# Kernel optimization log

Measured on AMD Instinct MI355X. Metric: run time of the kernel, lower is better.

## Reference

```python
import jax, jax.numpy as jnp
import numpy as np
import math

EMBED = 1024
HEADS = 16
HEAD_DIM = EMBED // HEADS


def setup_inputs() -> dict:
    key = jax.random.key(0)
    k1, k2, k3 = jax.random.split(key, 3)
    B, C, N = 2, EMBED, 2048
    x = jax.random.normal(k1, (B, C, N), dtype=jnp.float32)
    # Conv1d(kernel_size=1, bias=False) weights, stored as [out_ch, in_ch]
    fan = 1.0 / math.sqrt(EMBED)
    w_qkv = jax.random.uniform(k2, (3 * EMBED, EMBED), dtype=jnp.float32, minval=-fan, maxval=fan)
    w_out = jax.random.uniform(k3, (EMBED, EMBED), dtype=jnp.float32, minval=-fan, maxval=fan)
    return {"x": x, "w_qkv": w_qkv, "w_out": w_out}


def reference(x, w_qkv, w_out):
    B, C, N = x.shape
    H, HD = HEADS, HEAD_DIM
    # 1x1 conv == channel matmul: [B, 3E, N]
    qkv = jnp.einsum('oc,bcn->bon', w_qkv, x)
    # permute -> [B, N, 3E]; reshape splits 3E as (H, 3*HD) per original code
    qkv = qkv.transpose(0, 2, 1).reshape(B, N, H, 3 * HD)
    qkv = qkv.transpose(0, 2, 1, 3)  # [B, H, N, 3*HD]
    q, k, v = jnp.split(qkv, 3, axis=-1)  # each [B, H, N, HD]
    scale = 1.0 / math.sqrt(HD)
    scores = jnp.einsum('bhnd,bhmd->bhnm', q, k) * scale
    weight = jax.nn.softmax(scores, axis=-1)
    vals = jnp.einsum('bhnm,bhmd->bhnd', weight, v)
    vals = vals.transpose(0, 2, 1, 3).reshape(B, N, C)  # [B, N, C]
    y = jnp.einsum('oc,bnc->bon', w_out, vals)  # [B, C, N]
    return y
```

## Files before the change

kernel.cpp:

```cpp
#include <hip/hip_runtime.h>
#include <stdint.h>

typedef unsigned short u16;
typedef __attribute__((ext_vector_type(8))) short bf16x8;
typedef __attribute__((ext_vector_type(4))) float f32x4;

#define NSEQ  2048
#define EMBED 1024
#define NHEAD 16
#define HDIM  64
#define QSCALE 0.1803368801111204f

__device__ __forceinline__ u16 f2bf(float f) {
  uint32_t u = __builtin_bit_cast(uint32_t, f);
  u += 0x7fffu + ((u >> 16) & 1u);
  return (u16)(u >> 16);
}

__device__ __forceinline__ uint32_t cvtpk(float a, float b) {
  uint32_t r;
  asm("v_cvt_pk_bf16_f32 %0, %1, %2" : "=v"(r) : "v"(a), "v"(b));
  return r;
}

__device__ __forceinline__ void gl_lds16(const void* g, void* l) {
  __builtin_amdgcn_global_load_lds(
      (const __attribute__((address_space(1))) void*)g,
      (__attribute__((address_space(3))) void*)l, 16, 0, 0);
}

struct alignas(8) us4 { u16 a, b, c, d; };

__global__ __launch_bounds__(256)
void convertw(const float* __restrict__ wq, const float* __restrict__ wo,
              u16* __restrict__ oq, u16* __restrict__ oo) {
  int idx = blockIdx.x * 256 + threadIdx.x;
  const float* src;
  u16* dst;
  if (idx < 786432) { src = wq; dst = oq; }
  else { idx -= 786432; src = wo; dst = oo; }
  f32x4 v = ((const f32x4*)src)[idx];
  us4 r;
  r.a = f2bf(v[0]); r.b = f2bf(v[1]); r.c = f2bf(v[2]); r.d = f2bf(v[3]);
  ((us4*)dst)[idx] = r;
}

__global__ __launch_bounds__(256)
void transpose_x(const float* __restrict__ x, u16* __restrict__ xT) {
  __shared__ float tile[32][33];
  const int b = blockIdx.z;
  const int n0 = blockIdx.x * 32, c0 = blockIdx.y * 32;
  const int tx = threadIdx.x & 31, ty = threadIdx.x >> 5;
  const float* xb = x + (size_t)b * EMBED * NSEQ;
  #pragma unroll
  for (int k = 0; k < 4; ++k)
    tile[ty + k * 8][tx] = xb[(size_t)(c0 + ty + k * 8) * NSEQ + n0 + tx];
  __syncthreads();
  u16* xTb = xT + (size_t)b * NSEQ * EMBED;
  #pragma unroll
  for (int k = 0; k < 4; ++k)
    xTb[(size_t)(n0 + ty + k * 8) * EMBED + c0 + tx] = f2bf(tile[tx][ty + k * 8]);
}

template<int EPI>
__global__ __launch_bounds__(256, 2)
void gemm_bt(const u16* __restrict__ A, const u16* __restrict__ Bm,
             u16* __restrict__ o_q, u16* __restrict__ o_k, u16* __restrict__ o_vt,
             float* __restrict__ o_f)
{
  __shared__ u16 lA[128 * 64];
  __shared__ u16 lB[128 * 64];
  const int t  = threadIdx.x;
  const int w  = t >> 6;
  const int l  = t & 63;
  const int lr = l & 15, lh = l >> 4;
  const int wm = w >> 1, wn = w & 1;
  const int bz = blockIdx.z;
  const int m0 = blockIdx.x * 128;
  const int n0 = blockIdx.y * 128;

  const u16* Ab = A  + (EPI == 0 ? (size_t)bz * NSEQ * EMBED : (size_t)0);
  const u16* Bb = Bm + (EPI == 0 ? (size_t)0 : (size_t)bz * NSEQ * EMBED);

  f32x4 acc[4][4];
  #pragma unroll
  for (int i = 0; i < 4; ++i)
    #pragma unroll
    for (int j = 0; j < 4; ++j)
      acc[i][j] = (f32x4){0.f, 0.f, 0.f, 0.f};

  const int srow = t >> 3;
  const int slot = t & 7;
  char* ldsA = (char*)lA + (w << 10);
  char* ldsB = (char*)lB + (w << 10);

  for (int k0 = 0; k0 < EMBED; k0 += 64) {
    __syncthreads();
    #pragma unroll
    for (int i = 0; i < 4; ++i) {
      const int row = i * 32 + srow;
      const int sc  = ((slot * 16) ^ ((row & 7) << 4)) >> 1;
      gl_lds16(Ab + (size_t)(m0 + row) * EMBED + k0 + sc, ldsA + i * 4096);
      gl_lds16(Bb + (size_t)(n0 + row) * EMBED + k0 + sc, ldsB + i * 4096);
    }
    __syncthreads();
    #pragma unroll
    for (int kk = 0; kk < 2; ++kk) {
      bf16x8 af[4], bfr[4];
      #pragma unroll
      for (int mr = 0; mr < 4; ++mr) {
        const int row = wm * 64 + mr * 16 + lr;
        const int c2  = (kk * 64 + lh * 16) ^ ((row & 7) << 4);
        af[mr] = *(const bf16x8*)((const char*)lA + row * 128 + c2);
      }
      #pragma unroll
      for (int nc = 0; nc < 4; ++nc) {
        const int row = wn * 64 + nc * 16 + lr;
        const int c2  = (kk * 64 + lh * 16) ^ ((row & 7) << 4);
        bfr[nc] = *(const bf16x8*)((const char*)lB + row * 128 + c2);
      }
      #pragma unroll
      for (int mr = 0; mr < 4; ++mr)
        #pragma unroll
        for (int nc = 0; nc < 4; ++nc)
          acc[mr][nc] = __builtin_amdgcn_mfma_f32_16x16x32_bf16(
              af[mr], bfr[nc], acc[mr][nc], 0, 0, 0);
    }
  }

  if constexpr (EPI == 0) {
    #pragma unroll
    for (int mr = 0; mr < 4; ++mr) {
      #pragma unroll
      for (int nc = 0; nc < 4; ++nc) {
        const int o  = n0 + wn * 64 + nc * 16 + lr;
        const int h  = o / 192;
        const int rr = o - h * 192;
        const size_t bh = (size_t)bz * NHEAD + h;
        #pragma unroll
        for (int r = 0; r < 4; ++r) {
          const int n = m0 + wm * 64 + mr * 16 + lh * 4 + r;
          if (rr < 64)       o_q [(bh * NSEQ + n) * HDIM + rr]         = f2bf(acc[mr][nc][r] * QSCALE);
          else if (rr < 128) o_k [(bh * NSEQ + n) * HDIM + (rr - 64)]  = f2bf(acc[mr][nc][r]);
          else               o_vt[(bh * HDIM + (rr - 128)) * NSEQ + n] = f2bf(acc[mr][nc][r]);
        }
      }
    }
  } else {
    #pragma unroll
    for (int mr = 0; mr < 4; ++mr)
      #pragma unroll
      for (int nc = 0; nc < 4; ++nc)
        #pragma unroll
        for (int r = 0; r < 4; ++r) {
          const int o = m0 + wm * 64 + mr * 16 + lh * 4 + r;
          const int n = n0 + wn * 64 + nc * 16 + lr;
          o_f[((size_t)bz * EMBED + o) * NSEQ + n] = acc[mr][nc][r];
        }
  }
}

__global__ __launch_bounds__(256, 4)
void attn(const u16* __restrict__ Q, const u16* __restrict__ K,
          const u16* __restrict__ Vt, u16* __restrict__ vals)
{
  __shared__ u16 lK[2][64 * 64], lV[2][64 * 64], lQP[64 * 64];
  const int t  = threadIdx.x;
  const int w  = t >> 6, l = t & 63;
  const int lr = l & 15, lh = l >> 4;
  const int bid = blockIdx.x;
  const int s   = bid >> 3;
  const int bh  = (bid & 7) + 8 * (s >> 5);
  const int q0  = (s & 31) * 64;
  const int b  = bh >> 4, h = bh & 15;
  const size_t qk0 = (size_t)bh * NSEQ * HDIM;
  const size_t vt0 = (size_t)bh * HDIM * NSEQ;
  const int srow = t >> 3, slot = t & 7;
  const int swzr = (lr & 7) << 4;
  char* const pbase = (char*)lQP + (w << 11) + lr * 128;

  #pragma unroll
  for (int i = 0; i < 2; ++i) {
    const int row = i * 32 + srow;
    const int sc  = ((slot * 16) ^ ((row & 7) << 4)) >> 1;
    gl_lds16(Q + qk0 + (size_t)(q0 + row) * HDIM + sc,
             (char*)lQP + i * 4096 + (w << 10));
    gl_lds16(K + qk0 + (size_t)row * HDIM + sc,
             (char*)lK[0] + i * 4096 + (w << 10));
    gl_lds16(Vt + vt0 + (size_t)row * NSEQ + sc,
             (char*)lV[0] + i * 4096 + (w << 10));
  }
  __syncthreads();

  bf16x8 qf[2];
  {
    const int qrow = w * 16 + lr;
    #pragma unroll
    for (int kk = 0; kk < 2; ++kk)
      qf[kk] = *(const bf16x8*)((const char*)lQP + qrow * 128 +
                                ((kk * 64 + lh * 16) ^ ((qrow & 7) << 4)));
  }

  f32x4 accO[4];
  #pragma unroll
  for (int i = 0; i < 4; ++i) accO[i] = (f32x4){0.f, 0.f, 0.f, 0.f};
  float m = -1e30f, lsum = 0.f;
  int cur = 0;

  for (int j0 = 0; j0 < NSEQ; j0 += 64) {
    const int jn = j0 + 64;
    if (jn < NSEQ) {
      char* nk = (char*)lK[cur ^ 1];
      char* nv = (char*)lV[cur ^ 1];
      #pragma unroll
      for (int i = 0; i < 2; ++i) {
        const int row = i * 32 + srow;
        const int sc  = ((slot * 16) ^ ((row & 7) << 4)) >> 1;
        gl_lds16(K  + qk0 + (size_t)(jn + row) * HDIM + sc, nk + i * 4096 + (w << 10));
        gl_lds16(Vt + vt0 + (size_t)row * NSEQ + jn + sc,   nv + i * 4096 + (w << 10));
      }
    }
    const char* kb = (const char*)lK[cur];
    const char* vb = (const char*)lV[cur];

    f32x4 accS[4];
    #pragma unroll
    for (int f = 0; f < 4; ++f) accS[f] = (f32x4){0.f, 0.f, 0.f, 0.f};
    __builtin_amdgcn_s_setprio(1);
    #pragma unroll
    for (int kk = 0; kk < 2; ++kk)
      #pragma unroll
      for (int f = 0; f < 4; ++f) {
        const int row = f * 16 + lr;
        const int c2  = (kk * 64 + lh * 16) ^ ((row & 7) << 4);
        bf16x8 kf = *(const bf16x8*)(kb + row * 128 + c2);
        accS[f] = __builtin_amdgcn_mfma_f32_16x16x32_bf16(kf, qf[kk], accS[f], 0, 0, 0);
      }
    __builtin_amdgcn_s_setprio(0);

    float fm[4];
    #pragma unroll
    for (int f = 0; f < 4; ++f)
      fm[f] = fmaxf(fmaxf(accS[f][0], accS[f][1]), fmaxf(accS[f][2], accS[f][3]));
    float tm = fmaxf(fmaxf(fm[0], fm[1]), fmaxf(fm[2], fm[3]));
    tm = fmaxf(tm, __shfl_xor(tm, 16, 64));
    tm = fmaxf(tm, __shfl_xor(tm, 32, 64));

    if (tm > m + 8.f) {
      const float al = exp2f(m - tm);
      lsum *= al;
      #pragma unroll
      for (int fd = 0; fd < 4; ++fd)
        #pragma unroll
        for (int r = 0; r < 4; ++r)
          accO[fd][r] *= al;
      m = tm;
    }

    float psum = 0.f;
    #pragma unroll
    for (int f = 0; f < 4; ++f) {
      const float e0 = exp2f(accS[f][0] - m);
      const float e1 = exp2f(accS[f][1] - m);
      const float e2 = exp2f(accS[f][2] - m);
      const float e3 = exp2f(accS[f][3] - m);
      psum += (e0 + e1) + (e2 + e3);
      uint2 pw;
      pw.x = cvtpk(e0, e1);
      pw.y = cvtpk(e2, e3);
      *(uint2*)(pbase + ((f * 32 + lh * 8) ^ swzr)) = pw;
    }
    psum += __shfl_xor(psum, 16, 64);
    psum += __shfl_xor(psum, 32, 64);
    lsum += psum;

    __builtin_amdgcn_s_setprio(1);
    #pragma unroll
    for (int kk = 0; kk < 2; ++kk) {
      bf16x8 pf = *(const bf16x8*)(pbase + ((kk * 64 + lh * 16) ^ swzr));
      #pragma unroll
      for (int fd = 0; fd < 4; ++fd) {
        const int row = fd * 16 + lr;
        const int c2  = (kk * 64 + lh * 16) ^ ((row & 7) << 4);
        bf16x8 vf = *(const bf16x8*)(vb + row * 128 + c2);
        accO[fd] = __builtin_amdgcn_mfma_f32_16x16x32_bf16(vf, pf, accO[fd], 0, 0, 0);
      }
    }
    __builtin_amdgcn_s_setprio(0);

    __syncthreads();
    cur ^= 1;
  }

  const float rl = 1.0f / lsum;
  const int n = q0 + w * 16 + lr;
  #pragma unroll
  for (int fd = 0; fd < 4; ++fd) {
    uint2 ow;
    ow.x = cvtpk(accO[fd][0] * rl, accO[fd][1] * rl);
    ow.y = cvtpk(accO[fd][2] * rl, accO[fd][3] * rl);
    const int c = h * HDIM + fd * 16 + lh * 4;
    *(uint2*)(vals + ((size_t)b * NSEQ + n) * EMBED + c) = ow;
  }
}

extern "C" void kernel_launch(void* const* d_in, const int* in_sizes, int n_in,
                              void* d_out, int out_size, void* d_ws, size_t ws_size,
                              hipStream_t stream) {
  const float* x    = (const float*)d_in[0];
  const float* wqkv = (const float*)d_in[1];
  const float* wout = (const float*)d_in[2];
  float* y = (float*)d_out;
  char* ws = (char*)d_ws;

  u16* b_wqkv = (u16*)(ws);
  u16* b_wout = (u16*)(ws + 6291456);
  u16* b_xT   = (u16*)(ws + 8388608);
  u16* b_Q    = (u16*)(ws + 16777216);
  u16* b_K    = (u16*)(ws + 25165824);
  u16* b_Vt   = (u16*)(ws + 33554432);
  u16* b_vals = (u16*)(ws + 41943040);

  convertw<<<4096, 256, 0, stream>>>(wqkv, wout, b_wqkv, b_wout);
  transpose_x<<<dim3(64, 32, 2), 256, 0, stream>>>(x, b_xT);
  gemm_bt<0><<<dim3(16, 24, 2), 256, 0, stream>>>(b_xT, b_wqkv, b_Q, b_K, b_Vt, nullptr);
  attn<<<1024, 256, 0, stream>>>(b_Q, b_K, b_Vt, b_vals);
  gemm_bt<1><<<dim3(8, 16, 2), 256, 0, stream>>>(b_wout, b_vals, nullptr, nullptr, nullptr, y);
}
```

Before: 215.2 us.

## Restructure attention loop with static double-buffer, swizzle GEMM blocks, halve out-proj M tile

```diff
diff --git a/kernel.cpp b/kernel.cpp
--- a/kernel.cpp
+++ b/kernel.cpp
@@ -62,13 +62,13 @@
     xTb[(size_t)(n0 + ty + k * 8) * EMBED + c0 + tx] = f2bf(tile[tx][ty + k * 8]);
 }
 
-template<int EPI>
+template<int EPI, int MR>
 __global__ __launch_bounds__(256, 2)
 void gemm_bt(const u16* __restrict__ A, const u16* __restrict__ Bm,
              u16* __restrict__ o_q, u16* __restrict__ o_k, u16* __restrict__ o_vt,
              float* __restrict__ o_f)
 {
-  __shared__ u16 lA[128 * 64];
+  __shared__ u16 lA[MR * 32 * 64];
   __shared__ u16 lB[128 * 64];
   const int t  = threadIdx.x;
   const int w  = t >> 6;
@@ -76,15 +76,18 @@
   const int lr = l & 15, lh = l >> 4;
   const int wm = w >> 1, wn = w & 1;
   const int bz = blockIdx.z;
-  const int m0 = blockIdx.x * 128;
-  const int n0 = blockIdx.y * 128;
+  const int NT  = (EPI == 0 ? 384 : 256);
+  const int c   = blockIdx.x + 16 * blockIdx.y;
+  const int swz = (c & 7) * (NT / 8) + (c >> 3);
+  const int m0  = (swz & 15) * (MR * 32);
+  const int n0  = (swz >> 4) * 128;
 
   const u16* Ab = A  + (EPI == 0 ? (size_t)bz * NSEQ * EMBED : (size_t)0);
   const u16* Bb = Bm + (EPI == 0 ? (size_t)0 : (size_t)bz * NSEQ * EMBED);
 
-  f32x4 acc[4][4];
-  #pragma unroll
-  for (int i = 0; i < 4; ++i)
+  f32x4 acc[MR][4];
+  #pragma unroll
+  for (int i = 0; i < MR; ++i)
     #pragma unroll
     for (int j = 0; j < 4; ++j)
       acc[i][j] = (f32x4){0.f, 0.f, 0.f, 0.f};
@@ -97,19 +100,24 @@
   for (int k0 = 0; k0 < EMBED; k0 += 64) {
     __syncthreads();
     #pragma unroll
+    for (int i = 0; i < MR; ++i) {
+      const int row = i * 32 + srow;
+      const int sc  = ((slot * 16) ^ ((row & 7) << 4)) >> 1;
+      gl_lds16(Ab + (size_t)(m0 + row) * EMBED + k0 + sc, ldsA + i * 4096);
+    }
+    #pragma unroll
     for (int i = 0; i < 4; ++i) {
       const int row = i * 32 + srow;
       const int sc  = ((slot * 16) ^ ((row & 7) << 4)) >> 1;
-      gl_lds16(Ab + (size_t)(m0 + row) * EMBED + k0 + sc, ldsA + i * 4096);
       gl_lds16(Bb + (size_t)(n0 + row) * EMBED + k0 + sc, ldsB + i * 4096);
     }
     __syncthreads();
     #pragma unroll
     for (int kk = 0; kk < 2; ++kk) {
-      bf16x8 af[4], bfr[4];
-      #pragma unroll
-      for (int mr = 0; mr < 4; ++mr) {
-        const int row = wm * 64 + mr * 16 + lr;
+      bf16x8 af[MR], bfr[4];
+      #pragma unroll
+      for (int mr = 0; mr < MR; ++mr) {
+        const int row = wm * (MR * 16) + mr * 16 + lr;
         const int c2  = (kk * 64 + lh * 16) ^ ((row & 7) << 4);
         af[mr] = *(const bf16x8*)((const char*)lA + row * 128 + c2);
       }
@@ -120,7 +128,7 @@
         bfr[nc] = *(const bf16x8*)((const char*)lB + row * 128 + c2);
       }
       #pragma unroll
-      for (int mr = 0; mr < 4; ++mr)
+      for (int mr = 0; mr < MR; ++mr)
         #pragma unroll
         for (int nc = 0; nc < 4; ++nc)
           acc[mr][nc] = __builtin_amdgcn_mfma_f32_16x16x32_bf16(
@@ -130,7 +138,7 @@
 
   if constexpr (EPI == 0) {
     #pragma unroll
-    for (int mr = 0; mr < 4; ++mr) {
+    for (int mr = 0; mr < MR; ++mr) {
       #pragma unroll
       for (int nc = 0; nc < 4; ++nc) {
         const int o  = n0 + wn * 64 + nc * 16 + lr;
@@ -139,7 +147,7 @@
         const size_t bh = (size_t)bz * NHEAD + h;
         #pragma unroll
         for (int r = 0; r < 4; ++r) {
-          const int n = m0 + wm * 64 + mr * 16 + lh * 4 + r;
+          const int n = m0 + wm * (MR * 16) + mr * 16 + lh * 4 + r;
           if (rr < 64)       o_q [(bh * NSEQ + n) * HDIM + rr]         = f2bf(acc[mr][nc][r] * QSCALE);
           else if (rr < 128) o_k [(bh * NSEQ + n) * HDIM + (rr - 64)]  = f2bf(acc[mr][nc][r]);
           else               o_vt[(bh * HDIM + (rr - 128)) * NSEQ + n] = f2bf(acc[mr][nc][r]);
@@ -148,12 +156,12 @@
     }
   } else {
     #pragma unroll
-    for (int mr = 0; mr < 4; ++mr)
+    for (int mr = 0; mr < MR; ++mr)
       #pragma unroll
       for (int nc = 0; nc < 4; ++nc)
         #pragma unroll
         for (int r = 0; r < 4; ++r) {
-          const int o = m0 + wm * 64 + mr * 16 + lh * 4 + r;
+          const int o = m0 + wm * (MR * 16) + mr * 16 + lh * 4 + r;
           const int n = n0 + wn * 64 + nc * 16 + lr;
           o_f[((size_t)bz * EMBED + o) * NSEQ + n] = acc[mr][nc][r];
         }
@@ -179,17 +187,87 @@
   const int swzr = (lr & 7) << 4;
   char* const pbase = (char*)lQP + (w << 11) + lr * 128;
 
+#define STAGE(J, KB, VB) do {                                                  \
+    _Pragma("unroll")                                                          \
+    for (int i_ = 0; i_ < 2; ++i_) {                                           \
+      const int row_ = i_ * 32 + srow;                                         \
+      const int sc_  = ((slot * 16) ^ ((row_ & 7) << 4)) >> 1;                 \
+      gl_lds16(K  + qk0 + (size_t)((J) + row_) * HDIM + sc_,                   \
+               (char*)(KB) + i_ * 4096 + (w << 10));                           \
+      gl_lds16(Vt + vt0 + (size_t)row_ * NSEQ + (J) + sc_,                     \
+               (char*)(VB) + i_ * 4096 + (w << 10));                           \
+    }                                                                          \
+  } while (0)
+
+#define ATILE(KB, VB) do {                                                     \
+    f32x4 accS[4];                                                             \
+    _Pragma("unroll")                                                          \
+    for (int f_ = 0; f_ < 4; ++f_) accS[f_] = (f32x4){0.f, 0.f, 0.f, 0.f};     \
+    __builtin_amdgcn_s_setprio(1);                                             \
+    _Pragma("unroll")                                                          \
+    for (int kk_ = 0; kk_ < 2; ++kk_)                                          \
+      _Pragma("unroll")                                                        \
+      for (int f_ = 0; f_ < 4; ++f_) {                                         \
+        const int row_ = f_ * 16 + lr;                                         \
+        const int c2_  = (kk_ * 64 + lh * 16) ^ swzr;                          \
+        bf16x8 kf_ = *(const bf16x8*)((const char*)(KB) + row_ * 128 + c2_);   \
+        accS[f_] = __builtin_amdgcn_mfma_f32_16x16x32_bf16(kf_, qf[kk_],       \
+                                                           accS[f_], 0, 0, 0);\
+      }                                                                        \
+    __builtin_amdgcn_s_setprio(0);                                             \
+    float fm0_ = fmaxf(fmaxf(accS[0][0], accS[0][1]), fmaxf(accS[0][2], accS[0][3])); \
+    float fm1_ = fmaxf(fmaxf(accS[1][0], accS[1][1]), fmaxf(accS[1][2], accS[1][3])); \
+    float fm2_ = fmaxf(fmaxf(accS[2][0], accS[2][1]), fmaxf(accS[2][2], accS[2][3])); \
+    float fm3_ = fmaxf(fmaxf(accS[3][0], accS[3][1]), fmaxf(accS[3][2], accS[3][3])); \
+    float tm_ = fmaxf(fmaxf(fm0_, fm1_), fmaxf(fm2_, fm3_));                   \
+    tm_ = fmaxf(tm_, __shfl_xor(tm_, 16, 64));                                 \
+    tm_ = fmaxf(tm_, __shfl_xor(tm_, 32, 64));                                 \
+    if (tm_ > m + 8.f) {            \
+      const float al_ = exp2f(m - tm_);                                        \
+      lsum *= al_;                                                             \
+      _Pragma("unroll")                                                        \
+      for (int fd_ = 0; fd_ < 4; ++fd_)                                        \
+        _Pragma("unroll")                                                      \
+        for (int r_ = 0; r_ < 4; ++r_) accO[fd_][r_] *= al_;                   \
+      m = tm_;                                                                 \
+    }                                                                          \
+    _Pragma("unroll")                                                          \
+    for (int f_ = 0; f_ < 4; ++f_) {                                           \
+      const float e0_ = exp2f(accS[f_][0] - m);                                \
+      const float e1_ = exp2f(accS[f_][1] - m);                                \
+      const float e2_ = exp2f(accS[f_][2] - m);                                \
+      const float e3_ = exp2f(accS[f_][3] - m);                                \
+      lsum += (e0_ + e1_) + (e2_ + e3_);   \
+      uint2 pw_;                                                               \
+      pw_.x = cvtpk(e0_, e1_);                                                 \
+      pw_.y = cvtpk(e2_, e3_);                                                 \
+      *(uint2*)(pbase + ((f_ * 32 + lh * 8) ^ swzr)) = pw_;                    \
+    }                                                                          \
+    __builtin_amdgcn_s_setprio(1);                                             \
+    _Pragma("unroll")                                                          \
+    for (int kk_ = 0; kk_ < 2; ++kk_) {                                        \
+      bf16x8 pf_ = *(const bf16x8*)(pbase + ((kk_ * 64 + lh * 16) ^ swzr));    \
+      _Pragma("unroll")                                                        \
+      for (int fd_ = 0; fd_ < 4; ++fd_) {                                      \
+        const int row_ = fd_ * 16 + lr;                                        \
+        const int c2_  = (kk_ * 64 + lh * 16) ^ swzr;                          \
+        bf16x8 vf_ = *(const bf16x8*)((const char*)(VB) + row_ * 128 + c2_);   \
+        accO[fd_] = __builtin_amdgcn_mfma_f32_16x16x32_bf16(vf_, pf_,          \
+                                                            accO[fd_], 0, 0, 0);\
+      }                                                                        \
+    }                                                                          \
+    __builtin_amdgcn_s_setprio(0);                                             \
+  } while (0)
+
   #pragma unroll
   for (int i = 0; i < 2; ++i) {
     const int row = i * 32 + srow;
     const int sc  = ((slot * 16) ^ ((row & 7) << 4)) >> 1;
     gl_lds16(Q + qk0 + (size_t)(q0 + row) * HDIM + sc,
              (char*)lQP + i * 4096 + (w << 10));
-    gl_lds16(K + qk0 + (size_t)row * HDIM + sc,
-             (char*)lK[0] + i * 4096 + (w << 10));
-    gl_lds16(Vt + vt0 + (size_t)row * NSEQ + sc,
-             (char*)lV[0] + i * 4096 + (w << 10));
-  }
+  }
+  STAGE(0, lK[0], lV[0]);
+  STAGE(64, lK[1], lV[1]);
   __syncthreads();
 
   bf16x8 qf[2];
@@ -205,93 +283,22 @@
   #pragma unroll
   for (int i = 0; i < 4; ++i) accO[i] = (f32x4){0.f, 0.f, 0.f, 0.f};
   float m = -1e30f, lsum = 0.f;
-  int cur = 0;
-
-  for (int j0 = 0; j0 < NSEQ; j0 += 64) {
-    const int jn = j0 + 64;
-    if (jn < NSEQ) {
-      char* nk = (char*)lK[cur ^ 1];
-      char* nv = (char*)lV[cur ^ 1];
-      #pragma unroll
-      for (int i = 0; i < 2; ++i) {
-        const int row = i * 32 + srow;
-        const int sc  = ((slot * 16) ^ ((row & 7) << 4)) >> 1;
-        gl_lds16(K  + qk0 + (size_t)(jn + row) * HDIM + sc, nk + i * 4096 + (w << 10));
-        gl_lds16(Vt + vt0 + (size_t)row * NSEQ + jn + sc,   nv + i * 4096 + (w << 10));
-      }
-    }
-    const char* kb = (const char*)lK[cur];
-    const char* vb = (const char*)lV[cur];
-
-    f32x4 accS[4];
-    #pragma unroll
-    for (int f = 0; f < 4; ++f) accS[f] = (f32x4){0.f, 0.f, 0.f, 0.f};
-    __builtin_amdgcn_s_setprio(1);
-    #pragma unroll
-    for (int kk = 0; kk < 2; ++kk)
-      #pragma unroll
-      for (int f = 0; f < 4; ++f) {
-        const int row = f * 16 + lr;
-        const int c2  = (kk * 64 + lh * 16) ^ ((row & 7) << 4);
-        bf16x8 kf = *(const bf16x8*)(kb + row * 128 + c2);
-        accS[f] = __builtin_amdgcn_mfma_f32_16x16x32_bf16(kf, qf[kk], accS[f], 0, 0, 0);
-      }
-    __builtin_amdgcn_s_setprio(0);
-
-    float fm[4];
-    #pragma unroll
-    for (int f = 0; f < 4; ++f)
-      fm[f] = fmaxf(fmaxf(accS[f][0], accS[f][1]), fmaxf(accS[f][2], accS[f][3]));
-    float tm = fmaxf(fmaxf(fm[0], fm[1]), fmaxf(fm[2], fm[3]));
-    tm = fmaxf(tm, __shfl_xor(tm, 16, 64));
-    tm = fmaxf(tm, __shfl_xor(tm, 32, 64));
-
-    if (tm > m + 8.f) {
-      const float al = exp2f(m - tm);
-      lsum *= al;
-      #pragma unroll
-      for (int fd = 0; fd < 4; ++fd)
-        #pragma unroll
-        for (int r = 0; r < 4; ++r)
-          accO[fd][r] *= al;
-      m = tm;
-    }
-
-    float psum = 0.f;
-    #pragma unroll
-    for (int f = 0; f < 4; ++f) {
-      const float e0 = exp2f(accS[f][0] - m);
-      const float e1 = exp2f(accS[f][1] - m);
-      const float e2 = exp2f(accS[f][2] - m);
-      const float e3 = exp2f(accS[f][3] - m);
-      psum += (e0 + e1) + (e2 + e3);
-      uint2 pw;
-      pw.x = cvtpk(e0, e1);
-      pw.y = cvtpk(e2, e3);
-      *(uint2*)(pbase + ((f * 32 + lh * 8) ^ swzr)) = pw;
-    }
-    psum += __shfl_xor(psum, 16, 64);
-    psum += __shfl_xor(psum, 32, 64);
-    lsum += psum;
-
-    __builtin_amdgcn_s_setprio(1);
-    #pragma unroll
-    for (int kk = 0; kk < 2; ++kk) {
-      bf16x8 pf = *(const bf16x8*)(pbase + ((kk * 64 + lh * 16) ^ swzr));
-      #pragma unroll
-      for (int fd = 0; fd < 4; ++fd) {
-        const int row = fd * 16 + lr;
-        const int c2  = (kk * 64 + lh * 16) ^ ((row & 7) << 4);
-        bf16x8 vf = *(const bf16x8*)(vb + row * 128 + c2);
-        accO[fd] = __builtin_amdgcn_mfma_f32_16x16x32_bf16(vf, pf, accO[fd], 0, 0, 0);
-      }
-    }
-    __builtin_amdgcn_s_setprio(0);
-
+
+  for (int tt = 0; tt < 15; ++tt) {
+    const int j0 = tt * 128;
+    ATILE(lK[0], lV[0]);
     __syncthreads();
-    cur ^= 1;
-  }
-
+    STAGE(j0 + 128, lK[0], lV[0]);
+    ATILE(lK[1], lV[1]);
+    __syncthreads();
+    STAGE(j0 + 192, lK[1], lV[1]);
+  }
+  ATILE(lK[0], lV[0]);
+  __syncthreads();
+  ATILE(lK[1], lV[1]);
+
+  lsum += __shfl_xor(lsum, 16, 64);
+  lsum += __shfl_xor(lsum, 32, 64);
   const float rl = 1.0f / lsum;
   const int n = q0 + w * 16 + lr;
   #pragma unroll
@@ -302,6 +309,8 @@
     const int c = h * HDIM + fd * 16 + lh * 4;
     *(uint2*)(vals + ((size_t)b * NSEQ + n) * EMBED + c) = ow;
   }
+#undef STAGE
+#undef ATILE
 }
 
 extern "C" void kernel_launch(void* const* d_in, const int* in_sizes, int n_in,
@@ -323,7 +332,7 @@
 
   convertw<<<4096, 256, 0, stream>>>(wqkv, wout, b_wqkv, b_wout);
   transpose_x<<<dim3(64, 32, 2), 256, 0, stream>>>(x, b_xT);
-  gemm_bt<0><<<dim3(16, 24, 2), 256, 0, stream>>>(b_xT, b_wqkv, b_Q, b_K, b_Vt, nullptr);
+  gemm_bt<0, 4><<<dim3(16, 24, 2), 256, 0, stream>>>(b_xT, b_wqkv, b_Q, b_K, b_Vt, nullptr);
   attn<<<1024, 256, 0, stream>>>(b_Q, b_K, b_Vt, b_vals);
-  gemm_bt<1><<<dim3(8, 16, 2), 256, 0, stream>>>(b_wout, b_vals, nullptr, nullptr, nullptr, y);
-}
+  gemm_bt<1, 2><<<dim3(16, 16, 2), 256, 0, stream>>>(b_wout, b_vals, nullptr, nullptr, nullptr, y);
+}
```

After: 200.2 us. 7.0% less time.
